# Optimization experiments

Hardware: AMD Instinct MI355X
Metric: run time of the kernel (lower is better)

Reference implementation:

```python
import jax, jax.numpy as jnp
import numpy as np
from jax import lax

P = 8      # patch size (SGU hard-codes 8x8)
K = 7      # dynamic depthwise kernel size
EPS = 1e-5

def _gelu(x):
    return jax.nn.gelu(x, approximate=False)

def _ln_last(x, w, b):
    mu = jnp.mean(x, -1, keepdims=True)
    var = jnp.var(x, -1, keepdims=True)
    return (x - mu) / jnp.sqrt(var + EPS) * w + b

def _ln_chan(x, w, b):
    # WithBias LayerNorm over channel dim of an NCHW tensor (to_3d/to_4d)
    mu = jnp.mean(x, 1, keepdims=True)
    var = jnp.var(x, 1, keepdims=True)
    return (x - mu) / jnp.sqrt(var + EPS) * w[:, None, None] + b[:, None, None]

def _c1(x, w, b=None):
    # 1x1 conv on NCHW; w: (O, C)
    y = jnp.einsum('bchw,oc->bohw', x, w)
    return y if b is None else y + b[:, None, None]

def _dw3(x, w, b):
    # depthwise 3x3, padding 1; w: (C, 3, 3)
    C = x.shape[1]
    y = lax.conv_general_dilated(x, w[:, None], (1, 1), 'SAME',
        feature_group_count=C, dimension_numbers=('NCHW', 'OIHW', 'NCHW'))
    return y + b[:, None, None]

def _idynamic_dw(x, wdyn):
    # content-adaptive depthwise conv: x (B,C,P,P), per-position kernels
    # wdyn (B,K*K,P,P) shared across channels (groups = C // heads = 1)
    pad = K // 2
    xp = jnp.pad(x, ((0, 0), (0, 0), (pad, pad), (pad, pad)))
    out = jnp.zeros_like(x)
    for k in range(K * K):  # fixed small kernel loop, fused under jit
        i, j = divmod(k, K)
        out = out + xp[:, :, i:i + P, j:j + P] * wdyn[:, k][:, None]
    return out

def _forward(x, w_hid, b_hid, xcnn_w1, xcnn_b1, xcnn_ln_w, xcnn_ln_b,
             xcnn_dw_w, xcnn_dw_b, ci_w1, ci_b1, ci_ln_w, ci_ln_b, ci_w2, ci_b2,
             si_w1, si_b1, si_ln_w, si_ln_b, si_w2, si_b2,
             proj_w, proj_b, out_w, out_b, sgu_ln_w, sgu_ln_b,
             dwb_w0, idw_w1, idw_b1, idw_bn_w, idw_bn_b, idw_w2, idw_b2, dwb_w2):
    b, c, h, w = x.shape
    hh, ww = h // P, w // P
    n = hh * ww
    half = c // 2

    x = _gelu(_c1(x, w_hid, b_hid))
    # b c (hh P)(ww P) -> b hh ww p1 p2 c
    xp = x.reshape(b, c, hh, P, ww, P).transpose(0, 2, 4, 3, 5, 1)
    x_seq = xp.reshape(b, n, P * P, c)

    # x_cnn branch on (b*n, c, 8, 8) patch images
    xc = xp.reshape(b * n, P, P, c).transpose(0, 3, 1, 2)
    xc = _c1(xc, xcnn_w1, xcnn_b1)
    xc = _ln_chan(xc, xcnn_ln_w, xcnn_ln_b)
    xc = _gelu(_dw3(xc, xcnn_dw_w, xcnn_dw_b))

    # channel interaction SE gate -> (b*n, c//2, 1, 1)
    pooled = jnp.mean(xc, (2, 3), keepdims=True)
    cdw = _c1(pooled, ci_w1, ci_b1)
    cdw = _gelu(_ln_chan(cdw, ci_ln_w, ci_ln_b))
    cdw = jax.nn.sigmoid(_c1(cdw, ci_w2, ci_b2))

    # SpatialGatingUnit
    res = x_seq[..., :half].reshape(b * n, P * P, half)
    gate = x_seq[..., half:].reshape(b * n, P * P, half)
    gate = gate * cdw.reshape(b * n, 1, half)
    gate = _ln_last(gate, sgu_ln_w, sgu_ln_b)
    g = gate.reshape(b * n, P, P, half).transpose(0, 3, 1, 2)
    g = _c1(g, dwb_w0)
    # IDynamicDWConv kernel generation (1x1 -> BN(eval, stats 0/1) -> ReLU -> 1x1)
    t = _c1(g, idw_w1, idw_b1)
    t = t / jnp.sqrt(1.0 + EPS) * idw_bn_w[:, None, None] + idw_bn_b[:, None, None]
    t = jax.nn.relu(t)
    wdyn = _c1(t, idw_w2, idw_b2)  # (b*n, K*K, 8, 8)
    g = _idynamic_dw(g, wdyn)
    g = _c1(g, dwb_w2)
    gate = g.transpose(0, 2, 3, 1).reshape(b * n, P * P, half)
    x_sgu = gate * res  # act = Identity

    # stitch patches back to full resolution
    xc_full = xc.reshape(b, hh, ww, c, P, P).transpose(0, 3, 1, 4, 2, 5).reshape(b, c, h, w)
    x_att = x_sgu.reshape(b, hh, ww, P, P, half).transpose(0, 5, 1, 3, 2, 4).reshape(b, half, h, w)

    # spatial interaction gate (b,1,h,w)
    si = _c1(x_att, si_w1, si_b1)
    si = _gelu(_ln_chan(si, si_ln_w, si_ln_b))
    si = jax.nn.sigmoid(_c1(si, si_w2, si_b2))

    xproj = _c1(xc_full, proj_w, proj_b) * si
    out = jnp.concatenate([xproj, x_att], axis=1)
    return _c1(out, out_w, out_b)

def setup_inputs() -> dict:
    key = jax.random.key(0)
    ks = iter(jax.random.split(key, 40))
    dim, half = 64, 32
    B, H, W = 4, 256, 256
    def rn(shape):
        fan_in = int(np.prod(shape[1:])) if len(shape) > 1 else int(shape[0])
        return jax.random.normal(next(ks), shape, jnp.float32) / np.sqrt(fan_in)
    z = lambda n: jnp.zeros((n,), jnp.float32)
    o = lambda n: jnp.ones((n,), jnp.float32)
    return {
        'x': jax.random.normal(next(ks), (B, dim, H, W), jnp.float32),
        'w_hid': rn((dim, dim)), 'b_hid': z(dim),
        'xcnn_w1': rn((dim, dim)), 'xcnn_b1': z(dim),
        'xcnn_ln_w': o(dim), 'xcnn_ln_b': z(dim),
        'xcnn_dw_w': rn((dim, 3, 3)), 'xcnn_dw_b': z(dim),
        'ci_w1': rn((dim // 8, dim)), 'ci_b1': z(dim // 8),
        'ci_ln_w': o(dim // 8), 'ci_ln_b': z(dim // 8),
        'ci_w2': rn((half, dim // 8)), 'ci_b2': z(half),
        'si_w1': rn((dim // 16, half)), 'si_b1': z(dim // 16),
        'si_ln_w': o(dim // 16), 'si_ln_b': z(dim // 16),
        'si_w2': rn((1, dim // 16)), 'si_b2': z(1),
        'proj_w': rn((half, dim)), 'proj_b': z(half),
        'out_w': rn((dim, dim)), 'out_b': z(dim),
        'sgu_ln_w': o(half), 'sgu_ln_b': z(half),
        'dwb_w0': rn((half, half)),
        'idw_w1': rn((half // 4, half)), 'idw_b1': z(half // 4),
        'idw_bn_w': o(half // 4), 'idw_bn_b': z(half // 4),
        'idw_w2': rn((K * K, half // 4)), 'idw_b2': z(K * K),
        'dwb_w2': rn((half, half)),
    }

def reference(x, w_hid, b_hid, xcnn_w1, xcnn_b1, xcnn_ln_w, xcnn_ln_b,
              xcnn_dw_w, xcnn_dw_b, ci_w1, ci_b1, ci_ln_w, ci_ln_b, ci_w2, ci_b2,
              si_w1, si_b1, si_ln_w, si_ln_b, si_w2, si_b2,
              proj_w, proj_b, out_w, out_b, sgu_ln_w, sgu_ln_b,
              dwb_w0, idw_w1, idw_b1, idw_bn_w, idw_bn_b, idw_w2, idw_b2, dwb_w2):
    return _forward(x, w_hid, b_hid, xcnn_w1, xcnn_b1, xcnn_ln_w, xcnn_ln_b,
                    xcnn_dw_w, xcnn_dw_b, ci_w1, ci_b1, ci_ln_w, ci_ln_b, ci_w2, ci_b2,
                    si_w1, si_b1, si_ln_w, si_ln_b, si_w2, si_b2,
                    proj_w, proj_b, out_w, out_b, sgu_ln_w, sgu_ln_b,
                    dwb_w0, idw_w1, idw_b1, idw_bn_w, idw_bn_b, idw_w2, idw_b2, dwb_w2)
```

## Files before the change

### kernel.cpp

```cpp
#include <hip/hip_runtime.h>
#include <math.h>

#define HWSZ 65536
#define EPSF 1e-5f
#define PSTR 4680

typedef __attribute__((ext_vector_type(8))) short bf8v;
typedef __attribute__((ext_vector_type(4))) float f4v;
typedef __attribute__((ext_vector_type(4))) unsigned int u4v;
typedef unsigned int uint32;

#define W_HID_OFF   0
#define W_X1_OFF    4096
#define W_PROJ_OFF  8192
#define W_OUT_OFF   10240
#define W_DWB0_OFF  14336
#define W_DWB2_OFF  15360
#define F_DWT   0
#define F_CI1T  576
#define F_CI2T  1088
#define F_IW1T  1344
#define F_SI1T  1600

__device__ __forceinline__ float sigm(float v){ return 1.0f/(1.0f+expf(-v)); }
__device__ __forceinline__ float bl(uint32 u){ return __uint_as_float(u<<16); }
__device__ __forceinline__ float bh(uint32 u){ return __uint_as_float(u & 0xffff0000u); }
__device__ __forceinline__ uint32 pk2(float a, float b){
  uint32 r; asm("v_cvt_pk_bf16_f32 %0, %1, %2" : "=v"(r) : "v"(a), "v"(b)); return r;
}
__device__ __forceinline__ unsigned short bfr(float x){
  uint32 u = __float_as_uint(x); u += 0x7fffu + ((u>>16)&1u); return (unsigned short)(u>>16);
}
__device__ __forceinline__ float rcp_f(float x){ float r; asm("v_rcp_f32 %0, %1" : "=v"(r) : "v"(x)); return r; }
__device__ __forceinline__ float exp2_f(float x){ float r; asm("v_exp_f32 %0, %1" : "=v"(r) : "v"(x)); return r; }

__device__ __attribute__((noinline)) f4v gelu4(f4v v){
  f4v r;
  #pragma unroll
  for (int i=0;i<4;++i){
    float x  = v[i];
    float z  = fabsf(x) * 0.7071067811865476f;
    float t  = rcp_f(fmaf(0.3275911f, z, 1.0f));
    float p  = t*fmaf(t, fmaf(t, fmaf(t, fmaf(t, 1.061405429f, -1.453152027f),
                       1.421413741f), -0.284496736f), 0.254829592f);
    float ex = exp2_f(-(z*z)*1.4426950408889634f);
    float er = fmaf(-p, ex, 1.0f);
    float s  = copysignf(er, x);
    float hx = 0.5f*x;
    r[i] = fmaf(hx, s, hx);
  }
  return r;
}

#define WSYNC() asm volatile("s_waitcnt lgkmcnt(0)" ::: "memory")

__global__ void prep_w(const float* __restrict__ a0, const float* __restrict__ a1,
                       const float* __restrict__ a2, const float* __restrict__ a3,
                       const float* __restrict__ a4, const float* __restrict__ a5,
                       unsigned short* __restrict__ ws){
  int i = blockIdx.x*256 + threadIdx.x;
  if (i >= 16384) return;
  float v;
  if      (i < 4096)  v = a0[i];
  else if (i < 8192)  v = a1[i-4096];
  else if (i < 10240) v = a2[i-8192];
  else if (i < 14336) v = a3[i-10240];
  else if (i < 15360) v = a4[i-14336];
  else                v = a5[i-15360];
  ws[i] = bfr(v);
}

__global__ void prep_t(const float* __restrict__ dw, const float* __restrict__ ci1,
                       const float* __restrict__ ci2, const float* __restrict__ iw1,
                       const float* __restrict__ sw1, float* __restrict__ wf){
  int i = blockIdx.x*256 + threadIdx.x;
  if (i >= 1728) return;
  float v;
  if (i < 576)        { int k=i/64, c=i%64;            v = dw[c*9+k]; }
  else if (i < 1088)  { int j=i-576,  c=j/8, m=j%8;    v = ci1[m*64+c]; }
  else if (i < 1344)  { int j=i-1088, m=j/32, o=j%32;  v = ci2[o*8+m]; }
  else if (i < 1600)  { int j=i-1344, c=j/8, m=j%8;    v = iw1[m*32+c]; }
  else                { int j=i-1600, c=j/4, m=j%4;    v = sw1[m*32+c]; }
  wf[i] = v;
}

__global__ __launch_bounds__(256, 4)
void gmlp_fused(const float* __restrict__ x,
                const float* __restrict__ b_hid,
                const float* __restrict__ xcnn_b1,
                const float* __restrict__ xcnn_ln_w, const float* __restrict__ xcnn_ln_b,
                const float* __restrict__ xcnn_dw_b,
                const float* __restrict__ ci_b1,
                const float* __restrict__ ci_ln_w, const float* __restrict__ ci_ln_b,
                const float* __restrict__ ci_b2,
                const float* __restrict__ si_b1,
                const float* __restrict__ si_ln_w, const float* __restrict__ si_ln_b,
                const float* __restrict__ si_w2,   const float* __restrict__ si_b2,
                const float* __restrict__ proj_b,
                const float* __restrict__ out_b,
                const float* __restrict__ sgu_ln_w, const float* __restrict__ sgu_ln_b,
                const float* __restrict__ idw_b1,
                const float* __restrict__ idw_bn_w, const float* __restrict__ idw_bn_b,
                const float* __restrict__ idw_w2,  const float* __restrict__ idw_b2,
                const unsigned short* __restrict__ wsw,
                float* __restrict__ out)
{
    __shared__ __align__(16) unsigned short bufS[4*PSTR];
    __shared__ __align__(16) float segate_s[4][32];

    const float* wf = (const float*)wsw + 8192;

    const int tx  = threadIdx.x;
    const int wid = tx >> 6;
    const int t   = tx & 63;
    const int l4  = t & 15, g4 = t >> 4;
    const int py  = t >> 3,  px = t & 7;

    const int bid   = blockIdx.x;
    const int strip = bid & 7;
    const int ph    = (bid >> 3) & 31;
    const int bb    = bid >> 8;

    unsigned short* Wp = bufS + wid*PSTR;

    const int ty  = tx >> 5;
    const int txx = tx & 31;
    const int lp  = txx >> 3;
    const int lpx = txx & 7;
    const int yx  = ty*256 + txx;
    const float* xbase = x + (bb*64)*HWSZ + (ph*8)*256 + strip*32;
    unsigned short* ldst = bufS + lp*PSTR + (ty*8 + lpx)*72;

    #pragma unroll 1
    for (int c8 = 0; c8 < 8; ++c8) {
        u4v w;
        #pragma unroll
        for (int j = 0; j < 4; ++j) {
            int c = c8*8 + 2*j;
            float a = __builtin_nontemporal_load(xbase + c*HWSZ + yx);
            float b = __builtin_nontemporal_load(xbase + (c+1)*HWSZ + yx);
            w[j] = pk2(a, b);
        }
        *(u4v*)(ldst + c8*8) = w;
    }
    if (t < 9) *(u4v*)(Wp + 64*72 + t*8) = (u4v){0,0,0,0};
    __syncthreads();

    f4v acc[4][4];
    #pragma unroll
    for (int m = 0; m < 4; ++m)
        #pragma unroll
        for (int n = 0; n < 4; ++n)
            acc[m][n] = (f4v){0.f,0.f,0.f,0.f};
    #pragma unroll 1
    for (int s = 0; s < 2; ++s) {
        bf8v bw[4]; bf8v av[4];
        #pragma unroll
        for (int n = 0; n < 4; ++n) bw[n] = *(const bf8v*)(wsw + W_HID_OFF + (n*16+l4)*64 + s*32 + g4*8);
        #pragma unroll
        for (int m = 0; m < 4; ++m) av[m] = *(const bf8v*)(Wp + (m*16 + l4)*72 + s*32 + g4*8);
        #pragma unroll
        for (int m = 0; m < 4; ++m)
            #pragma unroll
            for (int n = 0; n < 4; ++n)
                acc[m][n] = __builtin_amdgcn_mfma_f32_16x16x32_bf16(av[m], bw[n], acc[m][n], 0,0,0);
    }
    {
        float bhid[4];
        #pragma unroll
        for (int n = 0; n < 4; ++n) bhid[n] = b_hid[n*16 + l4];
        #pragma unroll
        for (int m = 0; m < 4; ++m)
            #pragma unroll
            for (int n = 0; n < 4; ++n) {
                f4v q;
                #pragma unroll
                for (int r = 0; r < 4; ++r) q[r] = acc[m][n][r] + bhid[n];
                acc[m][n] = gelu4(q);
            }
    }
    WSYNC();
    #pragma unroll
    for (int m = 0; m < 4; ++m)
        #pragma unroll
        for (int n = 0; n < 4; ++n)
            #pragma unroll
            for (int r = 0; r < 4; ++r)
                Wp[(m*16 + g4*4 + r)*72 + n*16 + l4] = bfr(acc[m][n][r]);
    WSYNC();

    uint32 hidpk[32];
    #pragma unroll
    for (int q8 = 0; q8 < 8; ++q8) {
        u4v v = *(const u4v*)(Wp + t*72 + q8*8);
        #pragma unroll
        for (int j = 0; j < 4; ++j) hidpk[q8*4 + j] = v[j];
    }

    #pragma unroll
    for (int m = 0; m < 4; ++m)
        #pragma unroll
        for (int n = 0; n < 4; ++n)
            acc[m][n] = (f4v){0.f,0.f,0.f,0.f};
    #pragma unroll 1
    for (int s = 0; s < 2; ++s) {
        bf8v bw[4]; bf8v av[4];
        #pragma unroll
        for (int n = 0; n < 4; ++n) bw[n] = *(const bf8v*)(wsw + W_X1_OFF + (n*16+l4)*64 + s*32 + g4*8);
        #pragma unroll
        for (int m = 0; m < 4; ++m) av[m] = *(const bf8v*)(Wp + (m*16 + l4)*72 + s*32 + g4*8);
        #pragma unroll
        for (int m = 0; m < 4; ++m)
            #pragma unroll
            for (int n = 0; n < 4; ++n)
                acc[m][n] = __builtin_amdgcn_mfma_f32_16x16x32_bf16(av[m], bw[n], acc[m][n], 0,0,0);
    }
    {
        float bx[4];
        #pragma unroll
        for (int n = 0; n < 4; ++n) bx[n] = xcnn_b1[n*16 + l4];
        #pragma unroll
        for (int m = 0; m < 4; ++m)
            #pragma unroll
            for (int n = 0; n < 4; ++n)
                #pragma unroll
                for (int r = 0; r < 4; ++r)
                    acc[m][n][r] += bx[n];
    }
    WSYNC();
    #pragma unroll
    for (int m = 0; m < 4; ++m)
        #pragma unroll
        for (int n = 0; n < 4; ++n)
            #pragma unroll
            for (int r = 0; r < 4; ++r)
                Wp[(m*16 + g4*4 + r)*72 + n*16 + l4] = bfr(acc[m][n][r]);
    WSYNC();
    {
        float s = 0.f;
        #pragma unroll 1
        for (int q8 = 0; q8 < 8; ++q8) {
            u4v v = *(const u4v*)(Wp + t*72 + q8*8);
            #pragma unroll
            for (int j = 0; j < 4; ++j) s += bl(v[j]) + bh(v[j]);
        }
        float mu = s * (1.f/64.f);
        float s2 = 0.f;
        #pragma unroll 1
        for (int q8 = 0; q8 < 8; ++q8) {
            u4v v = *(const u4v*)(Wp + t*72 + q8*8);
            #pragma unroll
            for (int j = 0; j < 4; ++j) {
                float d0 = bl(v[j]) - mu, d1 = bh(v[j]) - mu;
                s2 = fmaf(d0, d0, fmaf(d1, d1, s2));
            }
        }
        float rstd = rsqrtf(s2*(1.f/64.f) + EPSF);
        #pragma unroll 1
        for (int q8 = 0; q8 < 8; ++q8) {
            u4v v = *(const u4v*)(Wp + t*72 + q8*8);
            u4v w;
            #pragma unroll
            for (int j = 0; j < 4; ++j) {
                int c = q8*8 + 2*j;
                float a = (bl(v[j]) - mu)*rstd*xcnn_ln_w[c]   + xcnn_ln_b[c];
                float b = (bh(v[j]) - mu)*rstd*xcnn_ln_w[c+1] + xcnn_ln_b[c+1];
                w[j] = pk2(a, b);
            }
            *(u4v*)(Wp + t*72 + q8*8) = w;
        }
    }
    WSYNC();

    #pragma unroll 1
    for (int h = 0; h < 2; ++h) {
        float xh[32];
        #pragma unroll
        for (int o = 0; o < 32; ++o) xh[o] = xcnn_dw_b[h*32 + o];
        #pragma unroll 1
        for (int ki = 0; ki < 3; ++ki) {
            #pragma unroll 1
            for (int kj = 0; kj < 3; ++kj) {
                int rr = py + ki - 1, cc = px + kj - 1;
                bool val = ((unsigned)rr < 8u) && ((unsigned)cc < 8u);
                int pnn = val ? rr*8 + cc : 64;
                const unsigned short* rp = Wp + pnn*72 + h*32;
                const float* wp = wf + F_DWT + (ki*3+kj)*64 + h*32;
                #pragma unroll
                for (int c8 = 0; c8 < 4; ++c8) {
                    u4v v = *(const u4v*)(rp + c8*8);
                    #pragma unroll
                    for (int j = 0; j < 4; ++j) {
                        int c = c8*8 + 2*j;
                        xh[c]   = fmaf(bl(v[j]), wp[c],   xh[c]);
                        xh[c+1] = fmaf(bh(v[j]), wp[c+1], xh[c+1]);
                    }
                }
            }
        }
        #pragma unroll
        for (int g = 0; g < 8; ++g) {
            f4v q = (f4v){xh[4*g], xh[4*g+1], xh[4*g+2], xh[4*g+3]};
            q = gelu4(q);
            xh[4*g]=q[0]; xh[4*g+1]=q[1]; xh[4*g+2]=q[2]; xh[4*g+3]=q[3];
        }
        WSYNC();
        #pragma unroll
        for (int c8 = 0; c8 < 4; ++c8) {
            u4v w;
            #pragma unroll
            for (int j = 0; j < 4; ++j) w[j] = pk2(xh[c8*8+2*j], xh[c8*8+2*j+1]);
            *(u4v*)(Wp + t*72 + h*32 + c8*8) = w;
        }
    }
    WSYNC();

    float pc;
    {
        float ps = 0.f;
        #pragma unroll 1
        for (int p8 = 0; p8 < 8; ++p8) {
            #pragma unroll
            for (int q = 0; q < 8; ++q) ps += bl((uint32)Wp[(p8*8+q)*72 + t]);
        }
        pc = ps * (1.f/64.f);
    }
    f4v accp[4][2];
    #pragma unroll
    for (int m = 0; m < 4; ++m) { accp[m][0] = (f4v){0.f,0.f,0.f,0.f}; accp[m][1] = (f4v){0.f,0.f,0.f,0.f}; }
    #pragma unroll 1
    for (int s = 0; s < 2; ++s) {
        bf8v bw[2]; bf8v av[4];
        #pragma unroll
        for (int n = 0; n < 2; ++n) bw[n] = *(const bf8v*)(wsw + W_PROJ_OFF + (n*16+l4)*64 + s*32 + g4*8);
        #pragma unroll
        for (int m = 0; m < 4; ++m) av[m] = *(const bf8v*)(Wp + (m*16 + l4)*72 + s*32 + g4*8);
        #pragma unroll
        for (int m = 0; m < 4; ++m)
            #pragma unroll
            for (int n = 0; n < 2; ++n)
                accp[m][n] = __builtin_amdgcn_mfma_f32_16x16x32_bf16(av[m], bw[n], accp[m][n], 0,0,0);
    }
    {
        float bp0 = proj_b[l4], bp1 = proj_b[16 + l4];
        #pragma unroll
        for (int m = 0; m < 4; ++m)
            #pragma unroll
            for (int r = 0; r < 4; ++r) { accp[m][0][r] += bp0; accp[m][1][r] += bp1; }
    }
    WSYNC();
    #pragma unroll
    for (int m = 0; m < 4; ++m)
        #pragma unroll
        for (int n = 0; n < 2; ++n)
            #pragma unroll
            for (int r = 0; r < 4; ++r)
                Wp[(m*16 + g4*4 + r)*72 + n*16 + l4] = bfr(accp[m][n][r]);
    WSYNC();
    uint32 xppk[16];
    #pragma unroll
    for (int q8 = 0; q8 < 4; ++q8) {
        u4v v = *(const u4v*)(Wp + t*72 + q8*8);
        #pragma unroll
        for (int j = 0; j < 4; ++j) xppk[q8*4 + j] = v[j];
    }

    {
        float pt[8];
        {
            f4v wa = *(const f4v*)(wf + F_CI1T + t*8);
            f4v wb = *(const f4v*)(wf + F_CI1T + t*8 + 4);
            #pragma unroll
            for (int m = 0; m < 4; ++m) { pt[m] = wa[m]*pc; pt[4+m] = wb[m]*pc; }
        }
        #pragma unroll
        for (int st = 1; st < 64; st <<= 1)
            #pragma unroll
            for (int m = 0; m < 8; ++m) pt[m] += __shfl_xor(pt[m], st, 64);
        float t8[8];
        #pragma unroll
        for (int m = 0; m < 8; ++m) t8[m] = pt[m] + ci_b1[m];
        float s = 0.f;
        #pragma unroll
        for (int m = 0; m < 8; ++m) s += t8[m];
        float mu = s * 0.125f;
        float q2 = 0.f;
        #pragma unroll
        for (int m = 0; m < 8; ++m) { float d = t8[m]-mu; q2 = fmaf(d,d,q2); }
        float rstd = rsqrtf(q2*0.125f + EPSF);
        #pragma unroll
        for (int m = 0; m < 8; ++m) t8[m] = (t8[m]-mu)*rstd*ci_ln_w[m] + ci_ln_b[m];
        f4v qa = gelu4((f4v){t8[0],t8[1],t8[2],t8[3]});
        f4v qb = gelu4((f4v){t8[4],t8[5],t8[6],t8[7]});
        t8[0]=qa[0]; t8[1]=qa[1]; t8[2]=qa[2]; t8[3]=qa[3];
        t8[4]=qb[0]; t8[5]=qb[1]; t8[6]=qb[2]; t8[7]=qb[3];
        if (t < 32) {
            float a = ci_b2[t];
            #pragma unroll
            for (int m = 0; m < 8; ++m) a = fmaf(wf[F_CI2T + m*32 + t], t8[m], a);
            segate_s[wid][t] = sigm(a);
        }
    }
    WSYNC();
    float sg[32];
    #pragma unroll
    for (int g = 0; g < 8; ++g) {
        f4v e = *(const f4v*)&segate_s[wid][g*4];
        #pragma unroll
        for (int r = 0; r < 4; ++r) {
            int o = g*4 + r;
            uint32 pkv = hidpk[16 + o/2];
            float gv = (o & 1) ? bh(pkv) : bl(pkv);
            sg[o] = gv * e[r];
        }
    }
    {
        float s = 0.f;
        #pragma unroll
        for (int o = 0; o < 32; ++o) s += sg[o];
        float mu = s * (1.f/32.f);
        float q2 = 0.f;
        #pragma unroll
        for (int o = 0; o < 32; ++o) { float d = sg[o]-mu; q2 = fmaf(d,d,q2); }
        float rstd = rsqrtf(q2*(1.f/32.f) + EPSF);
        #pragma unroll
        for (int o = 0; o < 32; ++o) sg[o] = (sg[o]-mu)*rstd*sgu_ln_w[o] + sgu_ln_b[o];
    }
    WSYNC();
    #pragma unroll
    for (int c8 = 0; c8 < 4; ++c8) {
        u4v w;
        #pragma unroll
        for (int j = 0; j < 4; ++j) w[j] = pk2(sg[c8*8+2*j], sg[c8*8+2*j+1]);
        *(u4v*)(Wp + t*72 + c8*8) = w;
    }
    WSYNC();

    {
        f4v accg[4][2];
        #pragma unroll
        for (int m = 0; m < 4; ++m) { accg[m][0] = (f4v){0.f,0.f,0.f,0.f}; accg[m][1] = (f4v){0.f,0.f,0.f,0.f}; }
        bf8v bw[2]; bf8v av[4];
        #pragma unroll
        for (int n = 0; n < 2; ++n) bw[n] = *(const bf8v*)(wsw + W_DWB0_OFF + (n*16+l4)*32 + g4*8);
        #pragma unroll
        for (int m = 0; m < 4; ++m) av[m] = *(const bf8v*)(Wp + (m*16 + l4)*72 + g4*8);
        #pragma unroll
        for (int m = 0; m < 4; ++m)
            #pragma unroll
            for (int n = 0; n < 2; ++n)
                accg[m][n] = __builtin_amdgcn_mfma_f32_16x16x32_bf16(av[m], bw[n], accg[m][n], 0,0,0);
        WSYNC();
        #pragma unroll
        for (int m = 0; m < 4; ++m)
            #pragma unroll
            for (int n = 0; n < 2; ++n)
                #pragma unroll
                for (int r = 0; r < 4; ++r) {
                    int q = m*16 + g4*4 + r;
                    Wp[((q>>5)*32 + n*16 + l4)*72 + 32 + (q & 31)] = bfr(accg[m][n][r]);
                }
    }
    WSYNC();

    float t8b[8];
    #pragma unroll
    for (int m = 0; m < 8; ++m) t8b[m] = idw_b1[m];
    #pragma unroll 1
    for (int c = 0; c < 32; ++c) {
        float gv = bl((uint32)Wp[((t>>5)*32 + c)*72 + 32 + (t & 31)]);
        #pragma unroll
        for (int m = 0; m < 8; ++m) t8b[m] = fmaf(wf[F_IW1T + c*8 + m], gv, t8b[m]);
    }
    #pragma unroll
    for (int m = 0; m < 8; ++m)
        t8b[m] = fmaxf(t8b[m]*(idw_bn_w[m]*0.9999950000374997f) + idw_bn_b[m], 0.f);

    f4v accd[4][2];
    #pragma unroll
    for (int m = 0; m < 4; ++m) { accd[m][0] = (f4v){0.f,0.f,0.f,0.f}; accd[m][1] = (f4v){0.f,0.f,0.f,0.f}; }
    #pragma unroll 1
    for (int s = 0; s < 2; ++s) {
        WSYNC();
        #pragma unroll
        for (int i = 0; i < 4; ++i) *(u4v*)(Wp + t*72 + i*8) = (u4v){0,0,0,0};
        #pragma unroll 1
        for (int ki = 0; ki < 7; ++ki) {
            int rr = py + ki - 3;
            #pragma unroll 1
            for (int kj = 0; kj < 7; ++kj) {
                int cc = px + kj - 3;
                int k  = ki*7 + kj;
                float wk = idw_b2[k];
                #pragma unroll
                for (int m = 0; m < 8; ++m) wk = fmaf(idw_w2[k*8 + m], t8b[m], wk);
                int q = rr*8 + cc;
                if (((unsigned)rr < 8u) && ((unsigned)cc < 8u) && ((q >> 5) == s))
                    Wp[t*72 + (q & 31)] = bfr(wk);
            }
        }
        WSYNC();
        bf8v aM[4], bG[2];
        #pragma unroll
        for (int m = 0; m < 4; ++m) aM[m] = *(const bf8v*)(Wp + (m*16 + l4)*72 + g4*8);
        #pragma unroll
        for (int n = 0; n < 2; ++n) bG[n] = *(const bf8v*)(Wp + (s*32 + n*16 + l4)*72 + 32 + g4*8);
        #pragma unroll
        for (int m = 0; m < 4; ++m)
            #pragma unroll
            for (int n = 0; n < 2; ++n)
                accd[m][n] = __builtin_amdgcn_mfma_f32_16x16x32_bf16(aM[m], bG[n], accd[m][n], 0,0,0);
    }
    WSYNC();
    #pragma unroll
    for (int m = 0; m < 4; ++m)
        #pragma unroll
        for (int n = 0; n < 2; ++n)
            #pragma unroll
            for (int r = 0; r < 4; ++r)
                Wp[(m*16 + g4*4 + r)*72 + n*16 + l4] = bfr(accd[m][n][r]);
    WSYNC();

    {
        f4v accg[4][2];
        #pragma unroll
        for (int m = 0; m < 4; ++m) { accg[m][0] = (f4v){0.f,0.f,0.f,0.f}; accg[m][1] = (f4v){0.f,0.f,0.f,0.f}; }
        bf8v bw[2]; bf8v av[4];
        #pragma unroll
        for (int n = 0; n < 2; ++n) bw[n] = *(const bf8v*)(wsw + W_DWB2_OFF + (n*16+l4)*32 + g4*8);
        #pragma unroll
        for (int m = 0; m < 4; ++m) av[m] = *(const bf8v*)(Wp + (m*16 + l4)*72 + g4*8);
        #pragma unroll
        for (int m = 0; m < 4; ++m)
            #pragma unroll
            for (int n = 0; n < 2; ++n)
                accg[m][n] = __builtin_amdgcn_mfma_f32_16x16x32_bf16(av[m], bw[n], accg[m][n], 0,0,0);
        WSYNC();
        #pragma unroll
        for (int m = 0; m < 4; ++m)
            #pragma unroll
            for (int n = 0; n < 2; ++n)
                #pragma unroll
                for (int r = 0; r < 4; ++r)
                    Wp[(m*16 + g4*4 + r)*72 + n*16 + l4] = bfr(accg[m][n][r]);
        WSYNC();
    }
    float sgu[32];
    #pragma unroll
    for (int q8 = 0; q8 < 4; ++q8) {
        u4v v = *(const u4v*)(Wp + t*72 + q8*8);
        #pragma unroll
        for (int j = 0; j < 4; ++j) {
            int q = q8*4 + j;
            sgu[2*q]   = bl(v[j]) * bl(hidpk[q]);
            sgu[2*q+1] = bh(v[j]) * bh(hidpk[q]);
        }
    }
    WSYNC();

    #pragma unroll
    for (int c8 = 0; c8 < 4; ++c8) {
        u4v w;
        #pragma unroll
        for (int j = 0; j < 4; ++j) w[j] = pk2(sgu[c8*8+2*j], sgu[c8*8+2*j+1]);
        *(u4v*)(Wp + t*72 + 32 + c8*8) = w;
    }
    WSYNC();
    float siv;
    {
        float s1[4];
        #pragma unroll
        for (int m = 0; m < 4; ++m) s1[m] = si_b1[m];
        #pragma unroll 1
        for (int c8 = 0; c8 < 4; ++c8) {
            u4v v = *(const u4v*)(Wp + t*72 + 32 + c8*8);
            #pragma unroll
            for (int j = 0; j < 4; ++j) {
                int c = c8*8 + 2*j;
                float a0 = bl(v[j]), a1 = bh(v[j]);
                #pragma unroll
                for (int m = 0; m < 4; ++m) {
                    s1[m] = fmaf(wf[F_SI1T + c*4 + m],     a0, s1[m]);
                    s1[m] = fmaf(wf[F_SI1T + (c+1)*4 + m], a1, s1[m]);
                }
            }
        }
        float s = s1[0]+s1[1]+s1[2]+s1[3];
        float mu = s * 0.25f;
        float q2 = 0.f;
        #pragma unroll
        for (int m = 0; m < 4; ++m) { float d = s1[m]-mu; q2 = fmaf(d,d,q2); }
        float rstd = rsqrtf(q2*0.25f + EPSF);
        f4v q;
        #pragma unroll
        for (int m = 0; m < 4; ++m) q[m] = (s1[m]-mu)*rstd*si_ln_w[m] + si_ln_b[m];
        q = gelu4(q);
        float a = si_b2[0];
        #pragma unroll
        for (int m = 0; m < 4; ++m) a = fmaf(si_w2[m], q[m], a);
        siv = sigm(a);
    }
    #pragma unroll
    for (int c8 = 0; c8 < 4; ++c8) {
        u4v w;
        #pragma unroll
        for (int j = 0; j < 4; ++j) {
            int q = c8*4 + j;
            w[j] = pk2(bl(xppk[q])*siv, bh(xppk[q])*siv);
        }
        *(u4v*)(Wp + t*72 + c8*8) = w;
    }
    WSYNC();

    #pragma unroll
    for (int m = 0; m < 4; ++m)
        #pragma unroll
        for (int n = 0; n < 4; ++n)
            acc[m][n] = (f4v){0.f,0.f,0.f,0.f};
    #pragma unroll 1
    for (int s = 0; s < 2; ++s) {
        bf8v bw[4]; bf8v av[4];
        #pragma unroll
        for (int n = 0; n < 4; ++n) bw[n] = *(const bf8v*)(wsw + W_OUT_OFF + (n*16+l4)*64 + s*32 + g4*8);
        #pragma unroll
        for (int m = 0; m < 4; ++m) av[m] = *(const bf8v*)(Wp + (m*16 + l4)*72 + s*32 + g4*8);
        #pragma unroll
        for (int m = 0; m < 4; ++m)
            #pragma unroll
            for (int n = 0; n < 4; ++n)
                acc[m][n] = __builtin_amdgcn_mfma_f32_16x16x32_bf16(av[m], bw[n], acc[m][n], 0,0,0);
    }
    {
        float bo[4];
        #pragma unroll
        for (int n = 0; n < 4; ++n) bo[n] = out_b[n*16 + l4];
        #pragma unroll
        for (int m = 0; m < 4; ++m)
            #pragma unroll
            for (int n = 0; n < 4; ++n)
                #pragma unroll
                for (int r = 0; r < 4; ++r)
                    acc[m][n][r] += bo[n];
    }
    WSYNC();
    #pragma unroll
    for (int m = 0; m < 4; ++m)
        #pragma unroll
        for (int n = 0; n < 4; ++n)
            #pragma unroll
            for (int r = 0; r < 4; ++r)
                Wp[(m*16 + g4*4 + r)*72 + n*16 + l4] = bfr(acc[m][n][r]);
    __syncthreads();

    {
        float* obase = out + (bb*64)*HWSZ + (ph*8)*256 + strip*32;
        const unsigned short* lsrc = bufS + lp*PSTR + (ty*8 + lpx)*72;
        #pragma unroll 1
        for (int c8 = 0; c8 < 8; ++c8) {
            u4v v = *(const u4v*)(lsrc + c8*8);
            #pragma unroll
            for (int j = 0; j < 4; ++j) {
                int c = c8*8 + 2*j;
                __builtin_nontemporal_store(bl(v[j]), obase + c*HWSZ + yx);
                __builtin_nontemporal_store(bh(v[j]), obase + (c+1)*HWSZ + yx);
            }
        }
    }
}

extern "C" void kernel_launch(void* const* d_in, const int* in_sizes, int n_in,
                              void* d_out, int out_size, void* d_ws, size_t ws_size,
                              hipStream_t stream) {
    const float* p[35];
    for (int i = 0; i < 35; ++i) p[i] = (const float*)d_in[i];
    unsigned short* ws = (unsigned short*)d_ws;
    float* wsf = (float*)ws + 8192;

    prep_w<<<64, 256, 0, stream>>>(p[1], p[3], p[21], p[23], p[27], p[34], ws);
    prep_t<<<7, 256, 0, stream>>>(p[7], p[9], p[13], p[28], p[15], wsf);

    const int B = in_sizes[0] / (64 * 256 * 256);
    dim3 grid(B * 32 * 8), block(256);
    gmlp_fused<<<grid, block, 0, stream>>>(
        p[0],  p[2],  p[4],  p[5],  p[6],  p[8],
        p[10], p[11], p[12], p[14],
        p[16], p[17], p[18], p[19], p[20],
        p[22], p[24], p[25], p[26],
        p[29], p[30], p[31], p[32], p[33],
        ws, (float*)d_out);
}
```

Before: 96.72 us.

## Process two patches per wave with 64-pixel strips and interleaved stages

Each block now covers a 64-pixel-wide strip (8 patches), so each wave handles two patches and every stage loops over both. Weight fragments are loaded once per stage and reused across both patches, the MFMA K-loop is unrolled, and the explicit LDS waitcnt barriers are removed. Sigmoid now uses hardware exp2/rcp. The grid halves, LDS per block doubles and launch bounds drop to 2 blocks per CU, which trades occupancy for more per-wave independent work and more register pressure (hpk/xppk arrays doubled).

```diff
diff --git a/kernel.cpp b/kernel.cpp
--- a/kernel.cpp
+++ b/kernel.cpp
@@ -22,7 +22,6 @@
 #define F_IW1T  1344
 #define F_SI1T  1600
 
-__device__ __forceinline__ float sigm(float v){ return 1.0f/(1.0f+expf(-v)); }
 __device__ __forceinline__ float bl(uint32 u){ return __uint_as_float(u<<16); }
 __device__ __forceinline__ float bh(uint32 u){ return __uint_as_float(u & 0xffff0000u); }
 __device__ __forceinline__ uint32 pk2(float a, float b){
@@ -33,6 +32,9 @@
 }
 __device__ __forceinline__ float rcp_f(float x){ float r; asm("v_rcp_f32 %0, %1" : "=v"(r) : "v"(x)); return r; }
 __device__ __forceinline__ float exp2_f(float x){ float r; asm("v_exp_f32 %0, %1" : "=v"(r) : "v"(x)); return r; }
+__device__ __forceinline__ float sigm(float v){
+  return rcp_f(1.0f + exp2_f(v * -1.4426950408889634f));
+}
 
 __device__ __attribute__((noinline)) f4v gelu4(f4v v){
   f4v r;
@@ -52,8 +54,6 @@
   return r;
 }
 
-#define WSYNC() asm volatile("s_waitcnt lgkmcnt(0)" ::: "memory")
-
 __global__ void prep_w(const float* __restrict__ a0, const float* __restrict__ a1,
                        const float* __restrict__ a2, const float* __restrict__ a3,
                        const float* __restrict__ a4, const float* __restrict__ a5,
@@ -84,7 +84,7 @@
   wf[i] = v;
 }
 
-__global__ __launch_bounds__(256, 4)
+__global__ __launch_bounds__(256, 2)
 void gmlp_fused(const float* __restrict__ x,
                 const float* __restrict__ b_hid,
                 const float* __restrict__ xcnn_b1,
@@ -105,8 +105,8 @@
                 const unsigned short* __restrict__ wsw,
                 float* __restrict__ out)
 {
-    __shared__ __align__(16) unsigned short bufS[4*PSTR];
-    __shared__ __align__(16) float segate_s[4][32];
+    __shared__ __align__(16) unsigned short bufS[8*PSTR];
+    __shared__ __align__(16) float segate_s[8][32];
 
     const float* wf = (const float*)wsw + 8192;
 
@@ -116,127 +116,129 @@
     const int l4  = t & 15, g4 = t >> 4;
     const int py  = t >> 3,  px = t & 7;
 
-    const int bid   = blockIdx.x;
-    const int strip = bid & 7;
-    const int ph    = (bid >> 3) & 31;
-    const int bb    = bid >> 8;
-
-    unsigned short* Wp = bufS + wid*PSTR;
+    const int bid = blockIdx.x;
+    const int s64 = bid & 3;
+    const int ph  = (bid >> 2) & 31;
+    const int bb  = bid >> 7;
 
     const int ty  = tx >> 5;
     const int txx = tx & 31;
-    const int lp  = txx >> 3;
-    const int lpx = txx & 7;
-    const int yx  = ty*256 + txx;
-    const float* xbase = x + (bb*64)*HWSZ + (ph*8)*256 + strip*32;
-    unsigned short* ldst = bufS + lp*PSTR + (ty*8 + lpx)*72;
+    const float* xbase = x + (bb*64)*HWSZ + (ph*8)*256 + s64*64;
 
     #pragma unroll 1
-    for (int c8 = 0; c8 < 8; ++c8) {
-        u4v w;
-        #pragma unroll
-        for (int j = 0; j < 4; ++j) {
-            int c = c8*8 + 2*j;
-            float a = __builtin_nontemporal_load(xbase + c*HWSZ + yx);
-            float b = __builtin_nontemporal_load(xbase + (c+1)*HWSZ + yx);
-            w[j] = pk2(a, b);
-        }
-        *(u4v*)(ldst + c8*8) = w;
-    }
-    if (t < 9) *(u4v*)(Wp + 64*72 + t*8) = (u4v){0,0,0,0};
+    for (int h = 0; h < 2; ++h) {
+        unsigned short* ldst = bufS + (h*4 + (txx>>3))*PSTR + (ty*8 + (txx&7))*72;
+        const float* xb = xbase + ty*256 + h*32 + txx;
+        #pragma unroll 2
+        for (int c8 = 0; c8 < 8; ++c8) {
+            u4v w;
+            #pragma unroll
+            for (int j = 0; j < 4; ++j) {
+                int c = c8*8 + 2*j;
+                w[j] = pk2(__builtin_nontemporal_load(xb + c*HWSZ),
+                           __builtin_nontemporal_load(xb + (c+1)*HWSZ));
+            }
+            *(u4v*)(ldst + c8*8) = w;
+        }
+    }
+    if (tx < 72) *(u4v*)(bufS + (tx/9)*PSTR + 64*72 + (tx%9)*8) = (u4v){0,0,0,0};
     __syncthreads();
 
-    f4v acc[4][4];
-    #pragma unroll
-    for (int m = 0; m < 4; ++m)
-        #pragma unroll
-        for (int n = 0; n < 4; ++n)
-            acc[m][n] = (f4v){0.f,0.f,0.f,0.f};
-    #pragma unroll 1
-    for (int s = 0; s < 2; ++s) {
-        bf8v bw[4]; bf8v av[4];
-        #pragma unroll
-        for (int n = 0; n < 4; ++n) bw[n] = *(const bf8v*)(wsw + W_HID_OFF + (n*16+l4)*64 + s*32 + g4*8);
-        #pragma unroll
-        for (int m = 0; m < 4; ++m) av[m] = *(const bf8v*)(Wp + (m*16 + l4)*72 + s*32 + g4*8);
+    uint32 hpk[2][32];
+    uint32 xppk[2][16];
+    float  pcv[2];
+
+    #pragma unroll
+    for (int p = 0; p < 2; ++p) {
+        unsigned short* Wp = bufS + (wid*2+p)*PSTR;
+        f4v acc[4][4];
+        #pragma unroll
+        for (int m = 0; m < 4; ++m)
+            #pragma unroll
+            for (int n = 0; n < 4; ++n) acc[m][n] = (f4v){0,0,0,0};
+        {
+            bf8v a0[4], a1[4];
+            #pragma unroll
+            for (int m = 0; m < 4; ++m) a0[m] = *(const bf8v*)(Wp + (m*16+l4)*72 + g4*8);
+            #pragma unroll
+            for (int m = 0; m < 4; ++m) a1[m] = *(const bf8v*)(Wp + (m*16+l4)*72 + 32 + g4*8);
+            #pragma unroll
+            for (int n = 0; n < 4; ++n) {
+                bf8v w0 = *(const bf8v*)(wsw + W_HID_OFF + (n*16+l4)*64 + g4*8);
+                bf8v w1 = *(const bf8v*)(wsw + W_HID_OFF + (n*16+l4)*64 + 32 + g4*8);
+                #pragma unroll
+                for (int m = 0; m < 4; ++m) {
+                    acc[m][n] = __builtin_amdgcn_mfma_f32_16x16x32_bf16(a0[m], w0, acc[m][n], 0,0,0);
+                    acc[m][n] = __builtin_amdgcn_mfma_f32_16x16x32_bf16(a1[m], w1, acc[m][n], 0,0,0);
+                }
+            }
+        }
+        #pragma unroll
+        for (int n = 0; n < 4; ++n) {
+            float bhid = b_hid[n*16 + l4];
+            #pragma unroll
+            for (int m = 0; m < 4; ++m) {
+                f4v q;
+                #pragma unroll
+                for (int r = 0; r < 4; ++r) q[r] = acc[m][n][r] + bhid;
+                acc[m][n] = gelu4(q);
+            }
+        }
         #pragma unroll
         for (int m = 0; m < 4; ++m)
             #pragma unroll
             for (int n = 0; n < 4; ++n)
-                acc[m][n] = __builtin_amdgcn_mfma_f32_16x16x32_bf16(av[m], bw[n], acc[m][n], 0,0,0);
-    }
-    {
-        float bhid[4];
-        #pragma unroll
-        for (int n = 0; n < 4; ++n) bhid[n] = b_hid[n*16 + l4];
-        #pragma unroll
-        for (int m = 0; m < 4; ++m)
+                #pragma unroll
+                for (int r = 0; r < 4; ++r)
+                    Wp[(m*16 + g4*4 + r)*72 + n*16 + l4] = bfr(acc[m][n][r]);
+        #pragma unroll
+        for (int q8 = 0; q8 < 8; ++q8) {
+            u4v v = *(const u4v*)(Wp + t*72 + q8*8);
+            #pragma unroll
+            for (int j = 0; j < 4; ++j) hpk[p][q8*4 + j] = v[j];
+        }
+    }
+
+    #pragma unroll
+    for (int p = 0; p < 2; ++p) {
+        unsigned short* Wp = bufS + (wid*2+p)*PSTR;
+        f4v acc[4][4];
+        #pragma unroll
+        for (int m = 0; m < 4; ++m)
+            #pragma unroll
+            for (int n = 0; n < 4; ++n) acc[m][n] = (f4v){0,0,0,0};
+        {
+            bf8v a0[4], a1[4];
+            #pragma unroll
+            for (int m = 0; m < 4; ++m) a0[m] = *(const bf8v*)(Wp + (m*16+l4)*72 + g4*8);
+            #pragma unroll
+            for (int m = 0; m < 4; ++m) a1[m] = *(const bf8v*)(Wp + (m*16+l4)*72 + 32 + g4*8);
             #pragma unroll
             for (int n = 0; n < 4; ++n) {
-                f4v q;
-                #pragma unroll
-                for (int r = 0; r < 4; ++r) q[r] = acc[m][n][r] + bhid[n];
-                acc[m][n] = gelu4(q);
-            }
-    }
-    WSYNC();
-    #pragma unroll
-    for (int m = 0; m < 4; ++m)
-        #pragma unroll
-        for (int n = 0; n < 4; ++n)
-            #pragma unroll
-            for (int r = 0; r < 4; ++r)
-                Wp[(m*16 + g4*4 + r)*72 + n*16 + l4] = bfr(acc[m][n][r]);
-    WSYNC();
-
-    uint32 hidpk[32];
-    #pragma unroll
-    for (int q8 = 0; q8 < 8; ++q8) {
-        u4v v = *(const u4v*)(Wp + t*72 + q8*8);
-        #pragma unroll
-        for (int j = 0; j < 4; ++j) hidpk[q8*4 + j] = v[j];
-    }
-
-    #pragma unroll
-    for (int m = 0; m < 4; ++m)
-        #pragma unroll
-        for (int n = 0; n < 4; ++n)
-            acc[m][n] = (f4v){0.f,0.f,0.f,0.f};
-    #pragma unroll 1
-    for (int s = 0; s < 2; ++s) {
-        bf8v bw[4]; bf8v av[4];
-        #pragma unroll
-        for (int n = 0; n < 4; ++n) bw[n] = *(const bf8v*)(wsw + W_X1_OFF + (n*16+l4)*64 + s*32 + g4*8);
-        #pragma unroll
-        for (int m = 0; m < 4; ++m) av[m] = *(const bf8v*)(Wp + (m*16 + l4)*72 + s*32 + g4*8);
+                bf8v w0 = *(const bf8v*)(wsw + W_X1_OFF + (n*16+l4)*64 + g4*8);
+                bf8v w1 = *(const bf8v*)(wsw + W_X1_OFF + (n*16+l4)*64 + 32 + g4*8);
+                #pragma unroll
+                for (int m = 0; m < 4; ++m) {
+                    acc[m][n] = __builtin_amdgcn_mfma_f32_16x16x32_bf16(a0[m], w0, acc[m][n], 0,0,0);
+                    acc[m][n] = __builtin_amdgcn_mfma_f32_16x16x32_bf16(a1[m], w1, acc[m][n], 0,0,0);
+                }
+            }
+        }
+        #pragma unroll
+        for (int n = 0; n < 4; ++n) {
+            float bx = xcnn_b1[n*16 + l4];
+            #pragma unroll
+            for (int m = 0; m < 4; ++m)
+                #pragma unroll
+                for (int r = 0; r < 4; ++r) acc[m][n][r] += bx;
+        }
         #pragma unroll
         for (int m = 0; m < 4; ++m)
             #pragma unroll
             for (int n = 0; n < 4; ++n)
-                acc[m][n] = __builtin_amdgcn_mfma_f32_16x16x32_bf16(av[m], bw[n], acc[m][n], 0,0,0);
-    }
-    {
-        float bx[4];
-        #pragma unroll
-        for (int n = 0; n < 4; ++n) bx[n] = xcnn_b1[n*16 + l4];
-        #pragma unroll
-        for (int m = 0; m < 4; ++m)
-            #pragma unroll
-            for (int n = 0; n < 4; ++n)
                 #pragma unroll
                 for (int r = 0; r < 4; ++r)
-                    acc[m][n][r] += bx[n];
-    }
-    WSYNC();
-    #pragma unroll
-    for (int m = 0; m < 4; ++m)
-        #pragma unroll
-        for (int n = 0; n < 4; ++n)
-            #pragma unroll
-            for (int r = 0; r < 4; ++r)
-                Wp[(m*16 + g4*4 + r)*72 + n*16 + l4] = bfr(acc[m][n][r]);
-    WSYNC();
-    {
+                    Wp[(m*16 + g4*4 + r)*72 + n*16 + l4] = bfr(acc[m][n][r]);
         float s = 0.f;
         #pragma unroll 1
         for (int q8 = 0; q8 < 8; ++q8) {
@@ -270,108 +272,115 @@
             *(u4v*)(Wp + t*72 + q8*8) = w;
         }
     }
-    WSYNC();
 
     #pragma unroll 1
-    for (int h = 0; h < 2; ++h) {
-        float xh[32];
-        #pragma unroll
-        for (int o = 0; o < 32; ++o) xh[o] = xcnn_dw_b[h*32 + o];
+    for (int p = 0; p < 2; ++p) {
+        unsigned short* Wp = bufS + (wid*2+p)*PSTR;
         #pragma unroll 1
-        for (int ki = 0; ki < 3; ++ki) {
+        for (int h = 0; h < 2; ++h) {
+            float xh[32];
+            #pragma unroll
+            for (int o = 0; o < 32; ++o) xh[o] = xcnn_dw_b[h*32 + o];
             #pragma unroll 1
-            for (int kj = 0; kj < 3; ++kj) {
-                int rr = py + ki - 1, cc = px + kj - 1;
-                bool val = ((unsigned)rr < 8u) && ((unsigned)cc < 8u);
-                int pnn = val ? rr*8 + cc : 64;
-                const unsigned short* rp = Wp + pnn*72 + h*32;
-                const float* wp = wf + F_DWT + (ki*3+kj)*64 + h*32;
-                #pragma unroll
-                for (int c8 = 0; c8 < 4; ++c8) {
-                    u4v v = *(const u4v*)(rp + c8*8);
+            for (int ki = 0; ki < 3; ++ki) {
+                #pragma unroll 1
+                for (int kj = 0; kj < 3; ++kj) {
+                    int rr = py + ki - 1, cc = px + kj - 1;
+                    bool val = ((unsigned)rr < 8u) && ((unsigned)cc < 8u);
+                    int pnn = val ? rr*8 + cc : 64;
+                    const unsigned short* rp = Wp + pnn*72 + h*32;
+                    const float* wpt = wf + F_DWT + (ki*3+kj)*64 + h*32;
                     #pragma unroll
-                    for (int j = 0; j < 4; ++j) {
-                        int c = c8*8 + 2*j;
-                        xh[c]   = fmaf(bl(v[j]), wp[c],   xh[c]);
-                        xh[c+1] = fmaf(bh(v[j]), wp[c+1], xh[c+1]);
+                    for (int c8 = 0; c8 < 4; ++c8) {
+                        u4v v = *(const u4v*)(rp + c8*8);
+                        #pragma unroll
+                        for (int j = 0; j < 4; ++j) {
+                            int c = c8*8 + 2*j;
+                            xh[c]   = fmaf(bl(v[j]), wpt[c],   xh[c]);
+                            xh[c+1] = fmaf(bh(v[j]), wpt[c+1], xh[c+1]);
+                        }
                     }
                 }
             }
-        }
-        #pragma unroll
-        for (int g = 0; g < 8; ++g) {
-            f4v q = (f4v){xh[4*g], xh[4*g+1], xh[4*g+2], xh[4*g+3]};
-            q = gelu4(q);
-            xh[4*g]=q[0]; xh[4*g+1]=q[1]; xh[4*g+2]=q[2]; xh[4*g+3]=q[3];
-        }
-        WSYNC();
-        #pragma unroll
-        for (int c8 = 0; c8 < 4; ++c8) {
-            u4v w;
-            #pragma unroll
-            for (int j = 0; j < 4; ++j) w[j] = pk2(xh[c8*8+2*j], xh[c8*8+2*j+1]);
-            *(u4v*)(Wp + t*72 + h*32 + c8*8) = w;
-        }
-    }
-    WSYNC();
-
-    float pc;
-    {
-        float ps = 0.f;
-        #pragma unroll 1
-        for (int p8 = 0; p8 < 8; ++p8) {
-            #pragma unroll
-            for (int q = 0; q < 8; ++q) ps += bl((uint32)Wp[(p8*8+q)*72 + t]);
-        }
-        pc = ps * (1.f/64.f);
-    }
-    f4v accp[4][2];
-    #pragma unroll
-    for (int m = 0; m < 4; ++m) { accp[m][0] = (f4v){0.f,0.f,0.f,0.f}; accp[m][1] = (f4v){0.f,0.f,0.f,0.f}; }
-    #pragma unroll 1
-    for (int s = 0; s < 2; ++s) {
-        bf8v bw[2]; bf8v av[4];
-        #pragma unroll
-        for (int n = 0; n < 2; ++n) bw[n] = *(const bf8v*)(wsw + W_PROJ_OFF + (n*16+l4)*64 + s*32 + g4*8);
-        #pragma unroll
-        for (int m = 0; m < 4; ++m) av[m] = *(const bf8v*)(Wp + (m*16 + l4)*72 + s*32 + g4*8);
+            #pragma unroll
+            for (int g = 0; g < 8; ++g) {
+                f4v q = (f4v){xh[4*g], xh[4*g+1], xh[4*g+2], xh[4*g+3]};
+                q = gelu4(q);
+                xh[4*g]=q[0]; xh[4*g+1]=q[1]; xh[4*g+2]=q[2]; xh[4*g+3]=q[3];
+            }
+            #pragma unroll
+            for (int c8 = 0; c8 < 4; ++c8) {
+                u4v w;
+                #pragma unroll
+                for (int j = 0; j < 4; ++j) w[j] = pk2(xh[c8*8+2*j], xh[c8*8+2*j+1]);
+                *(u4v*)(Wp + t*72 + h*32 + c8*8) = w;
+            }
+        }
+    }
+
+    #pragma unroll
+    for (int p = 0; p < 2; ++p) {
+        unsigned short* Wp = bufS + (wid*2+p)*PSTR;
+        {
+            float ps = 0.f;
+            #pragma unroll 1
+            for (int p8 = 0; p8 < 8; ++p8) {
+                #pragma unroll
+                for (int q = 0; q < 8; ++q) ps += bl((uint32)Wp[(p8*8+q)*72 + t]);
+            }
+            pcv[p] = ps * (1.f/64.f);
+        }
+        f4v accp[4][2];
+        #pragma unroll
+        for (int m = 0; m < 4; ++m) { accp[m][0] = (f4v){0,0,0,0}; accp[m][1] = (f4v){0,0,0,0}; }
+        {
+            bf8v a0[4], a1[4];
+            #pragma unroll
+            for (int m = 0; m < 4; ++m) a0[m] = *(const bf8v*)(Wp + (m*16+l4)*72 + g4*8);
+            #pragma unroll
+            for (int m = 0; m < 4; ++m) a1[m] = *(const bf8v*)(Wp + (m*16+l4)*72 + 32 + g4*8);
+            #pragma unroll
+            for (int n = 0; n < 2; ++n) {
+                bf8v w0 = *(const bf8v*)(wsw + W_PROJ_OFF + (n*16+l4)*64 + g4*8);
+                bf8v w1 = *(const bf8v*)(wsw + W_PROJ_OFF + (n*16+l4)*64 + 32 + g4*8);
+                #pragma unroll
+                for (int m = 0; m < 4; ++m) {
+                    accp[m][n] = __builtin_amdgcn_mfma_f32_16x16x32_bf16(a0[m], w0, accp[m][n], 0,0,0);
+                    accp[m][n] = __builtin_amdgcn_mfma_f32_16x16x32_bf16(a1[m], w1, accp[m][n], 0,0,0);
+                }
+            }
+        }
+        {
+            float bp0 = proj_b[l4], bp1 = proj_b[16 + l4];
+            #pragma unroll
+            for (int m = 0; m < 4; ++m)
+                #pragma unroll
+                for (int r = 0; r < 4; ++r) { accp[m][0][r] += bp0; accp[m][1][r] += bp1; }
+        }
         #pragma unroll
         for (int m = 0; m < 4; ++m)
             #pragma unroll
             for (int n = 0; n < 2; ++n)
-                accp[m][n] = __builtin_amdgcn_mfma_f32_16x16x32_bf16(av[m], bw[n], accp[m][n], 0,0,0);
-    }
-    {
-        float bp0 = proj_b[l4], bp1 = proj_b[16 + l4];
-        #pragma unroll
-        for (int m = 0; m < 4; ++m)
-            #pragma unroll
-            for (int r = 0; r < 4; ++r) { accp[m][0][r] += bp0; accp[m][1][r] += bp1; }
-    }
-    WSYNC();
-    #pragma unroll
-    for (int m = 0; m < 4; ++m)
-        #pragma unroll
-        for (int n = 0; n < 2; ++n)
-            #pragma unroll
-            for (int r = 0; r < 4; ++r)
-                Wp[(m*16 + g4*4 + r)*72 + n*16 + l4] = bfr(accp[m][n][r]);
-    WSYNC();
-    uint32 xppk[16];
-    #pragma unroll
-    for (int q8 = 0; q8 < 4; ++q8) {
-        u4v v = *(const u4v*)(Wp + t*72 + q8*8);
-        #pragma unroll
-        for (int j = 0; j < 4; ++j) xppk[q8*4 + j] = v[j];
-    }
-
-    {
+                #pragma unroll
+                for (int r = 0; r < 4; ++r)
+                    Wp[(m*16 + g4*4 + r)*72 + n*16 + l4] = bfr(accp[m][n][r]);
+        #pragma unroll
+        for (int q8 = 0; q8 < 4; ++q8) {
+            u4v v = *(const u4v*)(Wp + t*72 + q8*8);
+            #pragma unroll
+            for (int j = 0; j < 4; ++j) xppk[p][q8*4 + j] = v[j];
+        }
+    }
+
+    #pragma unroll
+    for (int p = 0; p < 2; ++p) {
+        unsigned short* Wp = bufS + (wid*2+p)*PSTR;
         float pt[8];
         {
             f4v wa = *(const f4v*)(wf + F_CI1T + t*8);
             f4v wb = *(const f4v*)(wf + F_CI1T + t*8 + 4);
             #pragma unroll
-            for (int m = 0; m < 4; ++m) { pt[m] = wa[m]*pc; pt[4+m] = wb[m]*pc; }
+            for (int m = 0; m < 4; ++m) { pt[m] = wa[m]*pcv[p]; pt[4+m] = wb[m]*pcv[p]; }
         }
         #pragma unroll
         for (int st = 1; st < 64; st <<= 1)
@@ -398,59 +407,55 @@
             float a = ci_b2[t];
             #pragma unroll
             for (int m = 0; m < 8; ++m) a = fmaf(wf[F_CI2T + m*32 + t], t8[m], a);
-            segate_s[wid][t] = sigm(a);
-        }
-    }
-    WSYNC();
-    float sg[32];
-    #pragma unroll
-    for (int g = 0; g < 8; ++g) {
-        f4v e = *(const f4v*)&segate_s[wid][g*4];
-        #pragma unroll
-        for (int r = 0; r < 4; ++r) {
-            int o = g*4 + r;
-            uint32 pkv = hidpk[16 + o/2];
-            float gv = (o & 1) ? bh(pkv) : bl(pkv);
-            sg[o] = gv * e[r];
-        }
-    }
-    {
-        float s = 0.f;
-        #pragma unroll
-        for (int o = 0; o < 32; ++o) s += sg[o];
-        float mu = s * (1.f/32.f);
-        float q2 = 0.f;
-        #pragma unroll
-        for (int o = 0; o < 32; ++o) { float d = sg[o]-mu; q2 = fmaf(d,d,q2); }
-        float rstd = rsqrtf(q2*(1.f/32.f) + EPSF);
-        #pragma unroll
-        for (int o = 0; o < 32; ++o) sg[o] = (sg[o]-mu)*rstd*sgu_ln_w[o] + sgu_ln_b[o];
-    }
-    WSYNC();
-    #pragma unroll
-    for (int c8 = 0; c8 < 4; ++c8) {
-        u4v w;
-        #pragma unroll
-        for (int j = 0; j < 4; ++j) w[j] = pk2(sg[c8*8+2*j], sg[c8*8+2*j+1]);
-        *(u4v*)(Wp + t*72 + c8*8) = w;
-    }
-    WSYNC();
-
-    {
+            segate_s[wid*2+p][t] = sigm(a);
+        }
+        float sg[32];
+        #pragma unroll
+        for (int g = 0; g < 8; ++g) {
+            f4v e = *(const f4v*)&segate_s[wid*2+p][g*4];
+            #pragma unroll
+            for (int r = 0; r < 4; ++r) {
+                int o = g*4 + r;
+                uint32 pkv = hpk[p][16 + o/2];
+                float gv = (o & 1) ? bh(pkv) : bl(pkv);
+                sg[o] = gv * e[r];
+            }
+        }
+        float ss = 0.f;
+        #pragma unroll
+        for (int o = 0; o < 32; ++o) ss += sg[o];
+        float mu2 = ss * (1.f/32.f);
+        float qq = 0.f;
+        #pragma unroll
+        for (int o = 0; o < 32; ++o) { float d = sg[o]-mu2; qq = fmaf(d,d,qq); }
+        float rstd2 = rsqrtf(qq*(1.f/32.f) + EPSF);
+        #pragma unroll
+        for (int o = 0; o < 32; ++o) sg[o] = (sg[o]-mu2)*rstd2*sgu_ln_w[o] + sgu_ln_b[o];
+        #pragma unroll
+        for (int c8 = 0; c8 < 4; ++c8) {
+            u4v w;
+            #pragma unroll
+            for (int j = 0; j < 4; ++j) w[j] = pk2(sg[c8*8+2*j], sg[c8*8+2*j+1]);
+            *(u4v*)(Wp + t*72 + c8*8) = w;
+        }
+    }
+
+    #pragma unroll
+    for (int p = 0; p < 2; ++p) {
+        unsigned short* Wp = bufS + (wid*2+p)*PSTR;
         f4v accg[4][2];
         #pragma unroll
-        for (int m = 0; m < 4; ++m) { accg[m][0] = (f4v){0.f,0.f,0.f,0.f}; accg[m][1] = (f4v){0.f,0.f,0.f,0.f}; }
-        bf8v bw[2]; bf8v av[4];
-        #pragma unroll
-        for (int n = 0; n < 2; ++n) bw[n] = *(const bf8v*)(wsw + W_DWB0_OFF + (n*16+l4)*32 + g4*8);
-        #pragma unroll
-        for (int m = 0; m < 4; ++m) av[m] = *(const bf8v*)(Wp + (m*16 + l4)*72 + g4*8);
-        #pragma unroll
-        for (int m = 0; m < 4; ++m)
-            #pragma unroll
-            for (int n = 0; n < 2; ++n)
-                accg[m][n] = __builtin_amdgcn_mfma_f32_16x16x32_bf16(av[m], bw[n], accg[m][n], 0,0,0);
-        WSYNC();
+        for (int m = 0; m < 4; ++m) { accg[m][0] = (f4v){0,0,0,0}; accg[m][1] = (f4v){0,0,0,0}; }
+        bf8v av[4];
+        #pragma unroll
+        for (int m = 0; m < 4; ++m) av[m] = *(const bf8v*)(Wp + (m*16+l4)*72 + g4*8);
+        #pragma unroll
+        for (int n = 0; n < 2; ++n) {
+            bf8v w0 = *(const bf8v*)(wsw + W_DWB0_OFF + (n*16+l4)*32 + g4*8);
+            #pragma unroll
+            for (int m = 0; m < 4; ++m)
+                accg[m][n] = __builtin_amdgcn_mfma_f32_16x16x32_bf16(av[m], w0, accg[m][n], 0,0,0);
+        }
         #pragma unroll
         for (int m = 0; m < 4; ++m)
             #pragma unroll
@@ -461,81 +466,81 @@
                     Wp[((q>>5)*32 + n*16 + l4)*72 + 32 + (q & 31)] = bfr(accg[m][n][r]);
                 }
     }
-    WSYNC();
-
-    float t8b[8];
-    #pragma unroll
-    for (int m = 0; m < 8; ++m) t8b[m] = idw_b1[m];
+
     #pragma unroll 1
-    for (int c = 0; c < 32; ++c) {
-        float gv = bl((uint32)Wp[((t>>5)*32 + c)*72 + 32 + (t & 31)]);
-        #pragma unroll
-        for (int m = 0; m < 8; ++m) t8b[m] = fmaf(wf[F_IW1T + c*8 + m], gv, t8b[m]);
-    }
-    #pragma unroll
-    for (int m = 0; m < 8; ++m)
-        t8b[m] = fmaxf(t8b[m]*(idw_bn_w[m]*0.9999950000374997f) + idw_bn_b[m], 0.f);
-
-    f4v accd[4][2];
-    #pragma unroll
-    for (int m = 0; m < 4; ++m) { accd[m][0] = (f4v){0.f,0.f,0.f,0.f}; accd[m][1] = (f4v){0.f,0.f,0.f,0.f}; }
-    #pragma unroll 1
-    for (int s = 0; s < 2; ++s) {
-        WSYNC();
-        #pragma unroll
-        for (int i = 0; i < 4; ++i) *(u4v*)(Wp + t*72 + i*8) = (u4v){0,0,0,0};
+    for (int p = 0; p < 2; ++p) {
+        unsigned short* Wp = bufS + (wid*2+p)*PSTR;
+        float t8b[8];
+        #pragma unroll
+        for (int m = 0; m < 8; ++m) t8b[m] = idw_b1[m];
         #pragma unroll 1
-        for (int ki = 0; ki < 7; ++ki) {
-            int rr = py + ki - 3;
+        for (int c = 0; c < 32; ++c) {
+            float gv = bl((uint32)Wp[((t>>5)*32 + c)*72 + 32 + (t & 31)]);
+            #pragma unroll
+            for (int m = 0; m < 8; ++m) t8b[m] = fmaf(wf[F_IW1T + c*8 + m], gv, t8b[m]);
+        }
+        #pragma unroll
+        for (int m = 0; m < 8; ++m)
+            t8b[m] = fmaxf(t8b[m]*(idw_bn_w[m]*0.9999950000374997f) + idw_bn_b[m], 0.f);
+
+        f4v accd[4][2];
+        #pragma unroll
+        for (int m = 0; m < 4; ++m) { accd[m][0] = (f4v){0,0,0,0}; accd[m][1] = (f4v){0,0,0,0}; }
+        #pragma unroll 1
+        for (int s = 0; s < 2; ++s) {
+            #pragma unroll
+            for (int i = 0; i < 4; ++i) *(u4v*)(Wp + t*72 + i*8) = (u4v){0,0,0,0};
             #pragma unroll 1
-            for (int kj = 0; kj < 7; ++kj) {
-                int cc = px + kj - 3;
-                int k  = ki*7 + kj;
-                float wk = idw_b2[k];
-                #pragma unroll
-                for (int m = 0; m < 8; ++m) wk = fmaf(idw_w2[k*8 + m], t8b[m], wk);
-                int q = rr*8 + cc;
-                if (((unsigned)rr < 8u) && ((unsigned)cc < 8u) && ((q >> 5) == s))
-                    Wp[t*72 + (q & 31)] = bfr(wk);
-            }
-        }
-        WSYNC();
-        bf8v aM[4], bG[2];
-        #pragma unroll
-        for (int m = 0; m < 4; ++m) aM[m] = *(const bf8v*)(Wp + (m*16 + l4)*72 + g4*8);
-        #pragma unroll
-        for (int n = 0; n < 2; ++n) bG[n] = *(const bf8v*)(Wp + (s*32 + n*16 + l4)*72 + 32 + g4*8);
+            for (int ki = 0; ki < 7; ++ki) {
+                int rr = py + ki - 3;
+                #pragma unroll 1
+                for (int kj = 0; kj < 7; ++kj) {
+                    int cc = px + kj - 3;
+                    int k  = ki*7 + kj;
+                    float wk = idw_b2[k];
+                    #pragma unroll
+                    for (int m = 0; m < 8; ++m) wk = fmaf(idw_w2[k*8 + m], t8b[m], wk);
+                    int q = rr*8 + cc;
+                    if (((unsigned)rr < 8u) && ((unsigned)cc < 8u) && ((q >> 5) == s))
+                        Wp[t*72 + (q & 31)] = bfr(wk);
+                }
+            }
+            bf8v aM[4], bG[2];
+            #pragma unroll
+            for (int m = 0; m < 4; ++m) aM[m] = *(const bf8v*)(Wp + (m*16+l4)*72 + g4*8);
+            #pragma unroll
+            for (int n = 0; n < 2; ++n) bG[n] = *(const bf8v*)(Wp + (s*32 + n*16 + l4)*72 + 32 + g4*8);
+            #pragma unroll
+            for (int m = 0; m < 4; ++m)
+                #pragma unroll
+                for (int n = 0; n < 2; ++n)
+                    accd[m][n] = __builtin_amdgcn_mfma_f32_16x16x32_bf16(aM[m], bG[n], accd[m][n], 0,0,0);
+        }
         #pragma unroll
         for (int m = 0; m < 4; ++m)
             #pragma unroll
             for (int n = 0; n < 2; ++n)
-                accd[m][n] = __builtin_amdgcn_mfma_f32_16x16x32_bf16(aM[m], bG[n], accd[m][n], 0,0,0);
-    }
-    WSYNC();
-    #pragma unroll
-    for (int m = 0; m < 4; ++m)
-        #pragma unroll
-        for (int n = 0; n < 2; ++n)
-            #pragma unroll
-            for (int r = 0; r < 4; ++r)
-                Wp[(m*16 + g4*4 + r)*72 + n*16 + l4] = bfr(accd[m][n][r]);
-    WSYNC();
-
-    {
+                #pragma unroll
+                for (int r = 0; r < 4; ++r)
+                    Wp[(m*16 + g4*4 + r)*72 + n*16 + l4] = bfr(accd[m][n][r]);
+    }
+
+    #pragma unroll
+    for (int p = 0; p < 2; ++p) {
+        unsigned short* Wp = bufS + (wid*2+p)*PSTR;
         f4v accg[4][2];
         #pragma unroll
-        for (int m = 0; m < 4; ++m) { accg[m][0] = (f4v){0.f,0.f,0.f,0.f}; accg[m][1] = (f4v){0.f,0.f,0.f,0.f}; }
-        bf8v bw[2]; bf8v av[4];
-        #pragma unroll
-        for (int n = 0; n < 2; ++n) bw[n] = *(const bf8v*)(wsw + W_DWB2_OFF + (n*16+l4)*32 + g4*8);
-        #pragma unroll
-        for (int m = 0; m < 4; ++m) av[m] = *(const bf8v*)(Wp + (m*16 + l4)*72 + g4*8);
-        #pragma unroll
-        for (int m = 0; m < 4; ++m)
-            #pragma unroll
-            for (int n = 0; n < 2; ++n)
-                accg[m][n] = __builtin_amdgcn_mfma_f32_16x16x32_bf16(av[m], bw[n], accg[m][n], 0,0,0);
-        WSYNC();
+        for (int m = 0; m < 4; ++m) { accg[m][0] = (f4v){0,0,0,0}; accg[m][1] = (f4v){0,0,0,0}; }
+        bf8v av[4];
+        #pragma unroll
+        for (int m = 0; m < 4; ++m) av[m] = *(const bf8v*)(Wp + (m*16+l4)*72 + g4*8);
+        #pragma unroll
+        for (int n = 0; n < 2; ++n) {
+            bf8v w0 = *(const bf8v*)(wsw + W_DWB2_OFF + (n*16+l4)*32 + g4*8);
+            #pragma unroll
+            for (int m = 0; m < 4; ++m)
+                accg[m][n] = __builtin_amdgcn_mfma_f32_16x16x32_bf16(av[m], w0, accg[m][n], 0,0,0);
+        }
         #pragma unroll
         for (int m = 0; m < 4; ++m)
             #pragma unroll
@@ -543,126 +548,126 @@
                 #pragma unroll
                 for (int r = 0; r < 4; ++r)
                     Wp[(m*16 + g4*4 + r)*72 + n*16 + l4] = bfr(accg[m][n][r]);
-        WSYNC();
-    }
-    float sgu[32];
-    #pragma unroll
-    for (int q8 = 0; q8 < 4; ++q8) {
-        u4v v = *(const u4v*)(Wp + t*72 + q8*8);
-        #pragma unroll
-        for (int j = 0; j < 4; ++j) {
-            int q = q8*4 + j;
-            sgu[2*q]   = bl(v[j]) * bl(hidpk[q]);
-            sgu[2*q+1] = bh(v[j]) * bh(hidpk[q]);
-        }
-    }
-    WSYNC();
-
-    #pragma unroll
-    for (int c8 = 0; c8 < 4; ++c8) {
-        u4v w;
-        #pragma unroll
-        for (int j = 0; j < 4; ++j) w[j] = pk2(sgu[c8*8+2*j], sgu[c8*8+2*j+1]);
-        *(u4v*)(Wp + t*72 + 32 + c8*8) = w;
-    }
-    WSYNC();
-    float siv;
+        #pragma unroll
+        for (int q8 = 0; q8 < 4; ++q8) {
+            u4v v = *(const u4v*)(Wp + t*72 + q8*8);
+            u4v w;
+            #pragma unroll
+            for (int j = 0; j < 4; ++j) {
+                int q = q8*4 + j;
+                w[j] = pk2(bl(v[j]) * bl(hpk[p][q]), bh(v[j]) * bh(hpk[p][q]));
+            }
+            *(u4v*)(Wp + t*72 + 32 + q8*8) = w;
+        }
+    }
+
+    #pragma unroll
+    for (int p = 0; p < 2; ++p) {
+        unsigned short* Wp = bufS + (wid*2+p)*PSTR;
+        float siv;
+        {
+            float s1[4];
+            #pragma unroll
+            for (int m = 0; m < 4; ++m) s1[m] = si_b1[m];
+            #pragma unroll 1
+            for (int c8 = 0; c8 < 4; ++c8) {
+                u4v v = *(const u4v*)(Wp + t*72 + 32 + c8*8);
+                #pragma unroll
+                for (int j = 0; j < 4; ++j) {
+                    int c = c8*8 + 2*j;
+                    float a0 = bl(v[j]), a1 = bh(v[j]);
+                    #pragma unroll
+                    for (int m = 0; m < 4; ++m) {
+                        s1[m] = fmaf(wf[F_SI1T + c*4 + m],     a0, s1[m]);
+                        s1[m] = fmaf(wf[F_SI1T + (c+1)*4 + m], a1, s1[m]);
+                    }
+                }
+            }
+            float s = s1[0]+s1[1]+s1[2]+s1[3];
+            float mu = s * 0.25f;
+            float q2 = 0.f;
+            #pragma unroll
+            for (int m = 0; m < 4; ++m) { float d = s1[m]-mu; q2 = fmaf(d,d,q2); }
+            float rstd = rsqrtf(q2*0.25f + EPSF);
+            f4v q;
+            #pragma unroll
+            for (int m = 0; m < 4; ++m) q[m] = (s1[m]-mu)*rstd*si_ln_w[m] + si_ln_b[m];
+            q = gelu4(q);
+            float a = si_b2[0];
+            #pragma unroll
+            for (int m = 0; m < 4; ++m) a = fmaf(si_w2[m], q[m], a);
+            siv = sigm(a);
+        }
+        #pragma unroll
+        for (int c8 = 0; c8 < 4; ++c8) {
+            u4v w;
+            #pragma unroll
+            for (int j = 0; j < 4; ++j) {
+                int q = c8*4 + j;
+                w[j] = pk2(bl(xppk[p][q])*siv, bh(xppk[p][q])*siv);
+            }
+            *(u4v*)(Wp + t*72 + c8*8) = w;
+        }
+    }
+
+    #pragma unroll
+    for (int p = 0; p < 2; ++p) {
+        unsigned short* Wp = bufS + (wid*2+p)*PSTR;
+        f4v acc[4][4];
+        #pragma unroll
+        for (int m = 0; m < 4; ++m)
+            #pragma unroll
+            for (int n = 0; n < 4; ++n) acc[m][n] = (f4v){0,0,0,0};
+        {
+            bf8v a0[4], a1[4];
+            #pragma unroll
+            for (int m = 0; m < 4; ++m) a0[m] = *(const bf8v*)(Wp + (m*16+l4)*72 + g4*8);
+            #pragma unroll
+            for (int m = 0; m < 4; ++m) a1[m] = *(const bf8v*)(Wp + (m*16+l4)*72 + 32 + g4*8);
+            #pragma unroll
+            for (int n = 0; n < 4; ++n) {
+                bf8v w0 = *(const bf8v*)(wsw + W_OUT_OFF + (n*16+l4)*64 + g4*8);
+                bf8v w1 = *(const bf8v*)(wsw + W_OUT_OFF + (n*16+l4)*64 + 32 + g4*8);
+                #pragma unroll
+                for (int m = 0; m < 4; ++m) {
+                    acc[m][n] = __builtin_amdgcn_mfma_f32_16x16x32_bf16(a0[m], w0, acc[m][n], 0,0,0);
+                    acc[m][n] = __builtin_amdgcn_mfma_f32_16x16x32_bf16(a1[m], w1, acc[m][n], 0,0,0);
+                }
+            }
+        }
+        #pragma unroll
+        for (int n = 0; n < 4; ++n) {
+            float bo = out_b[n*16 + l4];
+            #pragma unroll
+            for (int m = 0; m < 4; ++m)
+                #pragma unroll
+                for (int r = 0; r < 4; ++r) acc[m][n][r] += bo;
+        }
+        #pragma unroll
+        for (int m = 0; m < 4; ++m)
+            #pragma unroll
+            for (int n = 0; n < 4; ++n)
+                #pragma unroll
+                for (int r = 0; r < 4; ++r)
+                    Wp[(m*16 + g4*4 + r)*72 + n*16 + l4] = bfr(acc[m][n][r]);
+    }
+    __syncthreads();
+
     {
-        float s1[4];
-        #pragma unroll
-        for (int m = 0; m < 4; ++m) s1[m] = si_b1[m];
+        float* obase = out + (bb*64)*HWSZ + (ph*8)*256 + s64*64;
         #pragma unroll 1
-        for (int c8 = 0; c8 < 4; ++c8) {
-            u4v v = *(const u4v*)(Wp + t*72 + 32 + c8*8);
-            #pragma unroll
-            for (int j = 0; j < 4; ++j) {
-                int c = c8*8 + 2*j;
-                float a0 = bl(v[j]), a1 = bh(v[j]);
-                #pragma unroll
-                for (int m = 0; m < 4; ++m) {
-                    s1[m] = fmaf(wf[F_SI1T + c*4 + m],     a0, s1[m]);
-                    s1[m] = fmaf(wf[F_SI1T + (c+1)*4 + m], a1, s1[m]);
-                }
-            }
-        }
-        float s = s1[0]+s1[1]+s1[2]+s1[3];
-        float mu = s * 0.25f;
-        float q2 = 0.f;
-        #pragma unroll
-        for (int m = 0; m < 4; ++m) { float d = s1[m]-mu; q2 = fmaf(d,d,q2); }
-        float rstd = rsqrtf(q2*0.25f + EPSF);
-        f4v q;
-        #pragma unroll
-        for (int m = 0; m < 4; ++m) q[m] = (s1[m]-mu)*rstd*si_ln_w[m] + si_ln_b[m];
-        q = gelu4(q);
-        float a = si_b2[0];
-        #pragma unroll
-        for (int m = 0; m < 4; ++m) a = fmaf(si_w2[m], q[m], a);
-        siv = sigm(a);
-    }
-    #pragma unroll
-    for (int c8 = 0; c8 < 4; ++c8) {
-        u4v w;
-        #pragma unroll
-        for (int j = 0; j < 4; ++j) {
-            int q = c8*4 + j;
-            w[j] = pk2(bl(xppk[q])*siv, bh(xppk[q])*siv);
-        }
-        *(u4v*)(Wp + t*72 + c8*8) = w;
-    }
-    WSYNC();
-
-    #pragma unroll
-    for (int m = 0; m < 4; ++m)
-        #pragma unroll
-        for (int n = 0; n < 4; ++n)
-            acc[m][n] = (f4v){0.f,0.f,0.f,0.f};
-    #pragma unroll 1
-    for (int s = 0; s < 2; ++s) {
-        bf8v bw[4]; bf8v av[4];
-        #pragma unroll
-        for (int n = 0; n < 4; ++n) bw[n] = *(const bf8v*)(wsw + W_OUT_OFF + (n*16+l4)*64 + s*32 + g4*8);
-        #pragma unroll
-        for (int m = 0; m < 4; ++m) av[m] = *(const bf8v*)(Wp + (m*16 + l4)*72 + s*32 + g4*8);
-        #pragma unroll
-        for (int m = 0; m < 4; ++m)
-            #pragma unroll
-            for (int n = 0; n < 4; ++n)
-                acc[m][n] = __builtin_amdgcn_mfma_f32_16x16x32_bf16(av[m], bw[n], acc[m][n], 0,0,0);
-    }
-    {
-        float bo[4];
-        #pragma unroll
-        for (int n = 0; n < 4; ++n) bo[n] = out_b[n*16 + l4];
-        #pragma unroll
-        for (int m = 0; m < 4; ++m)
-            #pragma unroll
-            for (int n = 0; n < 4; ++n)
-                #pragma unroll
-                for (int r = 0; r < 4; ++r)
-                    acc[m][n][r] += bo[n];
-    }
-    WSYNC();
-    #pragma unroll
-    for (int m = 0; m < 4; ++m)
-        #pragma unroll
-        for (int n = 0; n < 4; ++n)
-            #pragma unroll
-            for (int r = 0; r < 4; ++r)
-                Wp[(m*16 + g4*4 + r)*72 + n*16 + l4] = bfr(acc[m][n][r]);
-    __syncthreads();
-
-    {
-        float* obase = out + (bb*64)*HWSZ + (ph*8)*256 + strip*32;
-        const unsigned short* lsrc = bufS + lp*PSTR + (ty*8 + lpx)*72;
-        #pragma unroll 1
-        for (int c8 = 0; c8 < 8; ++c8) {
-            u4v v = *(const u4v*)(lsrc + c8*8);
-            #pragma unroll
-            for (int j = 0; j < 4; ++j) {
-                int c = c8*8 + 2*j;
-                __builtin_nontemporal_store(bl(v[j]), obase + c*HWSZ + yx);
-                __builtin_nontemporal_store(bh(v[j]), obase + (c+1)*HWSZ + yx);
+        for (int h = 0; h < 2; ++h) {
+            const unsigned short* lsrc = bufS + (h*4 + (txx>>3))*PSTR + (ty*8 + (txx&7))*72;
+            float* ob = obase + ty*256 + h*32 + txx;
+            #pragma unroll 1
+            for (int c8 = 0; c8 < 8; ++c8) {
+                u4v v = *(const u4v*)(lsrc + c8*8);
+                #pragma unroll
+                for (int j = 0; j < 4; ++j) {
+                    int c = c8*8 + 2*j;
+                    __builtin_nontemporal_store(bl(v[j]), ob + c*HWSZ);
+                    __builtin_nontemporal_store(bh(v[j]), ob + (c+1)*HWSZ);
+                }
             }
         }
     }
@@ -680,7 +685,7 @@
     prep_t<<<7, 256, 0, stream>>>(p[7], p[9], p[13], p[28], p[15], wsf);
 
     const int B = in_sizes[0] / (64 * 256 * 256);
-    dim3 grid(B * 32 * 8), block(256);
+    dim3 grid(B * 32 * 4), block(256);
     gmlp_fused<<<grid, block, 0, stream>>>(
         p[0],  p[2],  p[4],  p[5],  p[6],  p[8],
         p[10], p[11], p[12], p[14],
```

New measurement: 112.5 us. 1.16x slower.
